# Optimization experiments

Measured on AMD Instinct MI355X. Metric: run time of the kernel, lower is better.

Reference implementation:

```python
import jax, jax.numpy as jnp
import numpy as np

VOCAB, HID, ADIM, B = 20, 128, 3, 32
NP, EP, NM, EM = 50000, 800000, 50000, 800000
IN_DIM = VOCAB + 3  # one-hot residues + 3D pos


def _gcn_conv(x, edge_index, W, b, n):
    # PyG GCNConv: h = XW; add self-loops; sym-normalized scatter-add; + bias
    h = x @ W
    loop = jnp.arange(n, dtype=edge_index.dtype)
    src = jnp.concatenate([edge_index[0], loop])
    dst = jnp.concatenate([edge_index[1], loop])
    deg = jax.ops.segment_sum(jnp.ones_like(dst, dtype=h.dtype), dst, num_segments=n)
    dinv = jnp.where(deg > 0, jax.lax.rsqrt(deg), 0.0)
    norm = dinv[src] * dinv[dst]  # [E+N]
    msg = h[src] * norm[:, None]  # [E+N, HID] dominant memory traffic
    return jax.ops.segment_sum(msg, dst, num_segments=n) + b


def _mean_pool(x, batch, nb):
    s = jax.ops.segment_sum(x, batch, num_segments=nb)
    c = jax.ops.segment_sum(jnp.ones((x.shape[0],), x.dtype), batch, num_segments=nb)
    return s / jnp.maximum(c, 1.0)[:, None]


def setup_inputs() -> dict:
    key = jax.random.key(0)
    ks = jax.random.split(key, 32)
    p = lambda k, shp: jax.random.normal(k, shp, dtype=jnp.float32) * 0.02
    inp = {
        "protein_residue": jax.random.randint(ks[0], (NP,), 0, VOCAB, dtype=jnp.int32),
        "protein_pos": jax.random.normal(ks[1], (NP, 3), dtype=jnp.float32),
        "protein_edge_index": jax.random.randint(ks[2], (2, EP), 0, NP, dtype=jnp.int32),
        "protein_batch": jnp.sort(jax.random.randint(ks[3], (NP,), 0, B, dtype=jnp.int32)),
        "molecule_residue": jax.random.randint(ks[4], (NM,), 0, VOCAB, dtype=jnp.int32),
        "molecule_pos": jax.random.normal(ks[5], (NM, 3), dtype=jnp.float32),
        "molecule_edge_index": jax.random.randint(ks[6], (2, EM), 0, NM, dtype=jnp.int32),
        "molecule_batch": jnp.sort(jax.random.randint(ks[7], (NM,), 0, B, dtype=jnp.int32)),
        "t": jax.random.randint(ks[8], (B,), 0, 1000, dtype=jnp.int32),
        "noisy_action": jax.random.normal(ks[9], (NM, ADIM), dtype=jnp.float32),
        # GCN params
        "Wp1": p(ks[10], (IN_DIM, HID)), "bp1": jnp.zeros((HID,), jnp.float32),
        "Wp2": p(ks[11], (HID, HID)),   "bp2": jnp.zeros((HID,), jnp.float32),
        "Wm1": p(ks[12], (IN_DIM, HID)), "bm1": jnp.zeros((HID,), jnp.float32),
        "Wm2": p(ks[13], (HID, HID)),   "bm2": jnp.zeros((HID,), jnp.float32),
        # timestep MLP
        "Wt1": p(ks[14], (1, HID)),   "bt1": jnp.zeros((HID,), jnp.float32),
        "Wt2": p(ks[15], (HID, HID)), "bt2": jnp.zeros((HID,), jnp.float32),
        # noise predictor: in = 2*HID + ADIM + HID = 387
        "Wn1": p(ks[16], (2 * HID + ADIM + HID, HID)), "bn1": jnp.zeros((HID,), jnp.float32),
        "Wn2": p(ks[17], (HID, ADIM)), "bn2": jnp.zeros((ADIM,), jnp.float32),
    }
    return inp


def reference(protein_residue, protein_pos, protein_edge_index, protein_batch,
              molecule_residue, molecule_pos, molecule_edge_index, molecule_batch,
              t, noisy_action,
              Wp1, bp1, Wp2, bp2, Wm1, bm1, Wm2, bm2,
              Wt1, bt1, Wt2, bt2, Wn1, bn1, Wn2, bn2):
    # protein branch
    x_p = jnp.concatenate([jax.nn.one_hot(protein_residue, VOCAB, dtype=jnp.float32), protein_pos], axis=1)
    x_p = jax.nn.relu(_gcn_conv(x_p, protein_edge_index, Wp1, bp1, NP))
    x_p = jax.nn.relu(_gcn_conv(x_p, protein_edge_index, Wp2, bp2, NP))
    protein_emb = _mean_pool(x_p, protein_batch, B)  # [B, HID]
    # molecule branch
    x_m = jnp.concatenate([jax.nn.one_hot(molecule_residue, VOCAB, dtype=jnp.float32), molecule_pos], axis=1)
    x_m = jax.nn.relu(_gcn_conv(x_m, molecule_edge_index, Wm1, bm1, NM))
    x_m = jax.nn.relu(_gcn_conv(x_m, molecule_edge_index, Wm2, bm2, NM))
    # timestep embedding
    t_emb = jax.nn.relu(t[:, None].astype(jnp.float32) @ Wt1 + bt1) @ Wt2 + bt2  # [B, HID]
    # gather pooled embeddings per molecule node, concat, MLP
    feat = jnp.concatenate([x_m, protein_emb[molecule_batch], t_emb[molecule_batch], noisy_action], axis=1)
    return jax.nn.relu(feat @ Wn1 + bn1) @ Wn2 + bn2  # [NM, ADIM]
```

## Files before the change

### kernel.cpp

```cpp
#include <hip/hip_runtime.h>
#include <hip/hip_bf16.h>

#define HID 128
#define BSH 7
#define CSRCAP 4096
#define PCHUNK 4096
#define HCHUNK 16384

typedef __attribute__((ext_vector_type(8))) short short8v;
typedef __attribute__((ext_vector_type(4))) float f32x4;

#if defined(__has_builtin)
#if __has_builtin(__builtin_amdgcn_cvt_f32_fp8) && __has_builtin(__builtin_amdgcn_cvt_pk_fp8_f32)
#define HAVE_HW_FP8 1
#endif
#endif

__device__ __forceinline__ float4 f4fma(float a, float4 x, float4 y) {
    y.x += a * x.x; y.y += a * x.y; y.z += a * x.z; y.w += a * x.w; return y;
}
__device__ __forceinline__ unsigned f2bf2(float lo, float hi) {
    unsigned ul = __float_as_uint(lo), uh = __float_as_uint(hi);
    ul = (ul + 0x7FFF + ((ul >> 16) & 1)) >> 16;
    uh = (uh + 0x7FFF + ((uh >> 16) & 1)) & 0xFFFF0000u;
    return ul | uh;
}
__device__ __forceinline__ unsigned short f2bf1(float v) {
    unsigned u = __float_as_uint(v);
    u = (u + 0x7FFF + ((u >> 16) & 1)) >> 16;
    return (unsigned short)u;
}
__device__ __forceinline__ float bflo(unsigned u) { return __uint_as_float(u << 16); }
__device__ __forceinline__ float bfhi(unsigned u) { return __uint_as_float(u & 0xFFFF0000u); }
__device__ __forceinline__ float bf2f(unsigned short b) {
    return __uint_as_float(((unsigned)b) << 16);
}
__device__ __forceinline__ short8v zero8() {
    short8v z = {0, 0, 0, 0, 0, 0, 0, 0};
    return z;
}

#ifndef HAVE_HW_FP8
__device__ __forceinline__ unsigned fp8enc_pos(float a) {
    if (a >= 448.f) return 0x7Eu;
    if (a < 0.0009765625f) return 0u;
    unsigned b = __float_as_uint(a);
    int e = (int)(b >> 23) - 127;
    if (e >= -6) {
        unsigned r = b + 0x7FFFFu + ((b >> 20) & 1u);
        e = (int)(r >> 23) - 127;
        unsigned m = (r >> 20) & 7u;
        return ((unsigned)(e + 7) << 3) | m;
    } else {
        int m = (int)(a * 512.f + 0.5f);
        return (unsigned)m;
    }
}
__device__ __forceinline__ float fp8dec1(unsigned u7) {
    float fn = __uint_as_float((u7 + 0x3C0u) << 20);
    float fs = (float)u7 * 0.001953125f;
    return u7 >= 8 ? fn : fs;
}
#endif

__device__ __forceinline__ unsigned enc4(float a, float b, float c, float d) {
#ifdef HAVE_HW_FP8
    int pk = __builtin_amdgcn_cvt_pk_fp8_f32(a, b, 0, false);
    pk = __builtin_amdgcn_cvt_pk_fp8_f32(c, d, pk, true);
    return (unsigned)pk;
#else
    return fp8enc_pos(a) | (fp8enc_pos(b) << 8) | (fp8enc_pos(c) << 16) | (fp8enc_pos(d) << 24);
#endif
}
__device__ __forceinline__ void dec8(uint2 u, float* v) {
#ifdef HAVE_HW_FP8
    v[0] = __builtin_amdgcn_cvt_f32_fp8((int)u.x, 0);
    v[1] = __builtin_amdgcn_cvt_f32_fp8((int)u.x, 1);
    v[2] = __builtin_amdgcn_cvt_f32_fp8((int)u.x, 2);
    v[3] = __builtin_amdgcn_cvt_f32_fp8((int)u.x, 3);
    v[4] = __builtin_amdgcn_cvt_f32_fp8((int)u.y, 0);
    v[5] = __builtin_amdgcn_cvt_f32_fp8((int)u.y, 1);
    v[6] = __builtin_amdgcn_cvt_f32_fp8((int)u.y, 2);
    v[7] = __builtin_amdgcn_cvt_f32_fp8((int)u.y, 3);
#else
    v[0] = fp8dec1(u.x & 0xffu);         v[1] = fp8dec1((u.x >> 8) & 0xffu);
    v[2] = fp8dec1((u.x >> 16) & 0xffu); v[3] = fp8dec1(u.x >> 24);
    v[4] = fp8dec1(u.y & 0xffu);         v[5] = fp8dec1((u.y >> 8) & 0xffu);
    v[6] = fp8dec1((u.y >> 16) & 0xffu); v[7] = fp8dec1(u.y >> 24);
#endif
}

__global__ __launch_bounds__(256) void k_bhist(const int* __restrict__ d1, int e1,
        const int* __restrict__ d2, int e2, int base2,
        int* __restrict__ bktcnt, long etot) {
    __shared__ int hist[1024];
    int tid = threadIdx.x;
    for (int b = tid; b < 1024; b += 256) hist[b] = 0;
    __syncthreads();
    long start = (long)blockIdx.x * HCHUNK;
    long end = start + HCHUNK; if (end > etot) end = etot;
    for (long i = start + tid; i < end; i += 256) {
        int d = (i < e1) ? d1[i] : d2[i - e1] + base2;
        atomicAdd(&hist[d >> BSH], 1);
    }
    __syncthreads();
    for (int b = tid; b < 1024; b += 256)
        if (hist[b]) atomicAdd(&bktcnt[b], hist[b]);
}

__global__ void k_bscan(const int* __restrict__ bktcnt, int* __restrict__ bofs,
                        int* __restrict__ bcur) {
    __shared__ int s[1024];
    int tid = threadIdx.x;
    int v = bktcnt[tid];
    s[tid] = v; __syncthreads();
    for (int o = 1; o < 1024; o <<= 1) {
        int t = (tid >= o) ? s[tid - o] : 0;
        __syncthreads();
        s[tid] += t;
        __syncthreads();
    }
    int ex = s[tid] - v;
    bofs[tid] = ex;
    bcur[tid] = ex;
    if (tid == 1023) bofs[1024] = s[1023];
}

__global__ __launch_bounds__(256) void k_part(
        const int* __restrict__ s1, const int* __restrict__ d1, int e1,
        const int* __restrict__ s2, const int* __restrict__ d2, int e2, int base2,
        int* __restrict__ bcur, int2* __restrict__ pedge, int nb, long etot) {
    __shared__ int hist[1024];
    __shared__ int lofs[1024];
    __shared__ int gb[1024];
    __shared__ int ps[256];
    __shared__ int2 stage[PCHUNK];
    __shared__ unsigned short sbk[PCHUNK];
    int tid = threadIdx.x;
    long cbase = (long)blockIdx.x * PCHUNK;
    int cnt = (int)((etot - cbase) < PCHUNK ? (etot - cbase) : PCHUNK);
    for (int b = tid; b < 1024; b += 256) hist[b] = 0;
    __syncthreads();
    for (int i = tid; i < cnt; i += 256) {
        long e = cbase + i;
        int d = (e < e1) ? d1[e] : d2[e - e1] + base2;
        atomicAdd(&hist[d >> BSH], 1);
    }
    __syncthreads();
    int h0 = hist[tid * 4], h1 = hist[tid * 4 + 1], h2 = hist[tid * 4 + 2], h3 = hist[tid * 4 + 3];
    int sum = h0 + h1 + h2 + h3;
    ps[tid] = sum; __syncthreads();
    for (int o = 1; o < 256; o <<= 1) {
        int v = (tid >= o) ? ps[tid - o] : 0;
        __syncthreads();
        ps[tid] += v;
        __syncthreads();
    }
    int ex = ps[tid] - sum;
    lofs[tid * 4] = ex; lofs[tid * 4 + 1] = ex + h0;
    lofs[tid * 4 + 2] = ex + h0 + h1; lofs[tid * 4 + 3] = ex + h0 + h1 + h2;
    __syncthreads();
    for (int b = tid; b < nb; b += 256) {
        int c = hist[b];
        gb[b] = c ? atomicAdd(&bcur[b], c) : 0;
    }
    __syncthreads();
    for (int b = tid; b < 1024; b += 256) hist[b] = 0;
    __syncthreads();
    for (int i = tid; i < cnt; i += 256) {
        long e = cbase + i;
        int s, d;
        if (e < e1) { s = s1[e]; d = d1[e]; }
        else { s = s2[e - e1] + base2; d = d2[e - e1] + base2; }
        int b = d >> BSH;
        int p = lofs[b] + atomicAdd(&hist[b], 1);
        stage[p] = make_int2(s, d);
        sbk[p] = (unsigned short)b;
    }
    __syncthreads();
    for (int i = tid; i < cnt; i += 256) {
        int b = sbk[i];
        pedge[gb[b] + (i - lofs[b])] = stage[i];
    }
}

__global__ __launch_bounds__(256) void k_csr(const int2* __restrict__ pe,
        const int* __restrict__ bofs, int* __restrict__ csrs,
        int* __restrict__ deg, int* __restrict__ offs, float* __restrict__ dinv,
        const int* __restrict__ res1, const float* __restrict__ pos1,
        const int* __restrict__ res2, const float* __restrict__ pos2,
        int np, int np64, uint4* __restrict__ nrec, int n) {
    __shared__ int lofs2[128];
    __shared__ int lcnt[128];
    __shared__ int lcur[128];
    __shared__ int sc[128];
    __shared__ int ss[CSRCAP];
    int b = blockIdx.x, tid = threadIdx.x;
    int n0 = b << BSH;
    int nn = (n - n0) < 128 ? (n - n0) : 128;
    if (tid < 128) { lcnt[tid] = 0; lcur[tid] = 0; }
    __syncthreads();
    int base = bofs[b], total = bofs[b + 1] - base;
    for (int i = tid; i < total; i += 256) atomicAdd(&lcnt[pe[base + i].y - n0], 1);
    __syncthreads();
    int v = 0;
    if (tid < 128) { v = lcnt[tid]; sc[tid] = v; }
    __syncthreads();
    for (int o = 1; o < 128; o <<= 1) {
        int t = 0;
        if (tid < 128 && tid >= o) t = sc[tid - o];
        __syncthreads();
        if (tid < 128) sc[tid] += t;
        __syncthreads();
    }
    if (tid < 128) lofs2[tid] = sc[tid] - v;
    if (tid < nn) {
        int node = n0 + tid;
        offs[node] = base + sc[tid] - v;
        deg[node] = v;
        float dv = rsqrtf((float)(v + 1));
        dinv[node] = dv;
        const int* res = 0; const float* pos = 0; int bseg = 0; bool valid = false;
        if (node < np) { res = res1; pos = pos1; bseg = 0; valid = true; }
        else if (node >= np64) { res = res2; pos = pos2; bseg = np64; valid = true; }
        if (valid) {
            int lg = node - bseg;
            uint4 rr;
            rr.x = __float_as_uint(dv);
            rr.y = (unsigned)res[lg] | ((unsigned)f2bf1(pos[lg * 3 + 0]) << 16);
            rr.z = (unsigned)f2bf1(pos[lg * 3 + 1]) | ((unsigned)f2bf1(pos[lg * 3 + 2]) << 16);
            rr.w = 0;
            nrec[node] = rr;
        }
    }
    __syncthreads();
    if (total <= CSRCAP) {
        for (int i = tid; i < total; i += 256) {
            int2 e = pe[base + i];
            int ln = e.y - n0;
            int pos_ = lofs2[ln] + atomicAdd(&lcur[ln], 1);
            ss[pos_] = e.x;
        }
        __syncthreads();
        for (int i = tid; i < total; i += 256) csrs[base + i] = ss[i];
    } else {
        for (int i = tid; i < total; i += 256) {
            int2 e = pe[base + i];
            int ln = e.y - n0;
            int pos_ = lofs2[ln] + atomicAdd(&lcur[ln], 1);
            csrs[base + pos_] = e.x;
        }
    }
}

__global__ __launch_bounds__(256) void k_agg23(
        const uint4* __restrict__ nrec, const int* __restrict__ offs,
        const int* __restrict__ deg, const int* __restrict__ csrs,
        int np, int np64, int nm,
        const float* __restrict__ W1a, const float* __restrict__ b1a,
        const float* __restrict__ W1b, const float* __restrict__ b1b,
        unsigned* __restrict__ xout) {
    __shared__ float agg[8][20];
    int grp = threadIdx.x >> 5, lane = threadIdx.x & 31;
    int g = blockIdx.x * 8 + grp;
    const float4 *W4, *bp;
    if (g < np) { W4 = (const float4*)W1a; bp = (const float4*)b1a; }
    else if (g >= np64 && g < np64 + nm) { W4 = (const float4*)W1b; bp = (const float4*)b1b; }
    else return;
    if (lane < 20) agg[grp][lane] = 0.f;
    float sx = 0.f, sy = 0.f, sz = 0.f;
    int s0 = offs[g], m = deg[g];
    for (int i = lane; i < m; i += 32) {
        int s = csrs[s0 + i];
        uint4 r = nrec[s];
        float dv = __uint_as_float(r.x);
        int rs = (int)(r.y & 0xffffu);
        float px = bfhi(r.y);
        float py = bflo(r.z);
        float pz = bfhi(r.z);
        atomicAdd(&agg[grp][rs], dv);
        sx += dv * px; sy += dv * py; sz += dv * pz;
    }
    #pragma unroll
    for (int o = 1; o < 32; o <<= 1) {
        sx += __shfl_xor(sx, o, 32);
        sy += __shfl_xor(sy, o, 32);
        sz += __shfl_xor(sz, o, 32);
    }
    uint4 sr = nrec[g];
    float dd = __uint_as_float(sr.x);
    int rsd = (int)(sr.y & 0xffffu);
    float spx = bfhi(sr.y), spy = bflo(sr.z), spz = bfhi(sr.z);
    float4 w20 = W4[20 * 32 + lane], w21 = W4[21 * 32 + lane], w22 = W4[22 * 32 + lane];
    float4 sm = W4[rsd * 32 + lane];
    sm = f4fma(spx, w20, sm); sm = f4fma(spy, w21, sm); sm = f4fma(spz, w22, sm);
    float4 acc = make_float4(dd * sm.x, dd * sm.y, dd * sm.z, dd * sm.w);
    #pragma unroll
    for (int r = 0; r < 20; ++r)
        acc = f4fma(agg[grp][r], W4[r * 32 + lane], acc);
    acc = f4fma(sx, w20, acc);
    acc = f4fma(sy, w21, acc);
    acc = f4fma(sz, w22, acc);
    float4 b = bp[lane];
    float s16 = 16.f * dd;
    float o0 = s16 * fmaxf(dd * acc.x + b.x, 0.f);
    float o1 = s16 * fmaxf(dd * acc.y + b.y, 0.f);
    float o2 = s16 * fmaxf(dd * acc.z + b.z, 0.f);
    float o3 = s16 * fmaxf(dd * acc.w + b.w, 0.f);
    xout[(size_t)g * 32 + lane] = enc4(o0, o1, o2, o3);
}

__global__ __launch_bounds__(256) void k_agg(
        const uint2* __restrict__ H8, const int* __restrict__ offs,
        const int* __restrict__ deg, const int* __restrict__ csrs,
        const float* __restrict__ dinv,
        int np, int np64, int nm,
        unsigned short* __restrict__ outb) {
    int g = blockIdx.x * 8 + (threadIdx.x >> 5);
    if (g >= np && (g < np64 || g >= np64 + nm)) return;
    int lane = threadIdx.x & 31;
    int half = lane >> 4, l15 = lane & 15;
    float acc[8];
    if (half == 0) {
        uint2 u = H8[(size_t)g * 16 + l15];
        float v[8]; dec8(u, v);
        #pragma unroll
        for (int c = 0; c < 8; ++c) acc[c] = v[c];
    } else {
        #pragma unroll
        for (int c = 0; c < 8; ++c) acc[c] = 0.f;
    }
    int s0 = offs[g], m = deg[g];
    int npair = (m + 1) >> 1;
    #pragma unroll 8
    for (int j = 0; j < npair; ++j) {
        int idx = 2 * j + half;
        bool act = idx < m;
        int s = csrs[s0 + (act ? idx : m - 1)];
        uint2 u = H8[(size_t)s * 16 + l15];
        float v[8]; dec8(u, v);
        if (act) {
            #pragma unroll
            for (int c = 0; c < 8; ++c) acc[c] += v[c];
        }
    }
    #pragma unroll
    for (int c = 0; c < 8; ++c) acc[c] += __shfl_xor(acc[c], 16, 32);
    if (half == 0) {
        float di = dinv[g] * 0.0625f;
        uint4 pk;
        pk.x = f2bf2(di * acc[0], di * acc[1]);
        pk.y = f2bf2(di * acc[2], di * acc[3]);
        pk.z = f2bf2(di * acc[4], di * acc[5]);
        pk.w = f2bf2(di * acc[6], di * acc[7]);
        *(uint4*)&outb[(size_t)g * HID + l15 * 8] = pk;
    }
}

__global__ void k_tr(const float* __restrict__ Wa, const float* __restrict__ Wb,
                     const float* __restrict__ Wc,
                     unsigned short* __restrict__ Ta, unsigned short* __restrict__ Tb,
                     unsigned short* __restrict__ Tc) {
    int b = blockIdx.x;
    int col = b & 127, m = b >> 7;
    const float* W = (m == 0) ? Wa : (m == 1 ? Wb : Wc);
    unsigned short* T = (m == 0) ? Ta : (m == 1 ? Tb : Tc);
    int k = threadIdx.x;
    T[col * HID + k] = f2bf1(W[k * HID + col]);
}

__global__ __launch_bounds__(256) void k_gemm(const unsigned short* __restrict__ A,
        const unsigned short* __restrict__ Bt1, const unsigned short* __restrict__ Bt2,
        const float* __restrict__ b2a, const float* __restrict__ b2b,
        int nb1, int np64, int ntot, unsigned short* __restrict__ C) {
    const int tid = threadIdx.x;
    const int wid = tid >> 6;
    const int lane = tid & 63;
    const int l15 = lane & 15, lg = lane >> 4;
    const unsigned short* Bt; const float* bb; int r0;
    if ((int)blockIdx.x < nb1) { Bt = Bt1; bb = b2a; r0 = blockIdx.x * 64; }
    else { Bt = Bt2; bb = b2b; r0 = np64 + ((int)blockIdx.x - nb1) * 64; }
    const int cbase = wid * 32;
    f32x4 acc[4][2] = {};
    #pragma unroll
    for (int ks = 0; ks < 4; ++ks) {
        int kb = ks * 32 + lg * 8;
        short8v b0 = *(const short8v*)&Bt[(size_t)(cbase + l15) * HID + kb];
        short8v b1 = *(const short8v*)&Bt[(size_t)(cbase + 16 + l15) * HID + kb];
        #pragma unroll
        for (int rt = 0; rt < 4; ++rt) {
            int gr = r0 + rt * 16 + l15;
            short8v a = (gr < ntot) ? *(const short8v*)&A[(size_t)gr * HID + kb] : zero8();
            acc[rt][0] = __builtin_amdgcn_mfma_f32_16x16x32_bf16(a, b0, acc[rt][0], 0, 0, 0);
            acc[rt][1] = __builtin_amdgcn_mfma_f32_16x16x32_bf16(a, b1, acc[rt][1], 0, 0, 0);
        }
    }
    float bc0 = bb[cbase + l15], bc1 = bb[cbase + 16 + l15];
    #pragma unroll
    for (int rt = 0; rt < 4; ++rt)
        #pragma unroll
        for (int i = 0; i < 4; ++i) {
            int gr = r0 + rt * 16 + lg * 4 + i;
            if (gr < ntot) {
                C[(size_t)gr * HID + cbase + l15]      = f2bf1(fmaxf(acc[rt][0][i] + bc0, 0.f));
                C[(size_t)gr * HID + cbase + 16 + l15] = f2bf1(fmaxf(acc[rt][1][i] + bc1, 0.f));
            }
        }
}

__global__ void k_pool(const unsigned short* __restrict__ x, const int* __restrict__ batch,
                       float* __restrict__ pool, int* __restrict__ cnt, int n) {
    const int ROWS = 64;
    int start = blockIdx.x * ROWS;
    if (start >= n) return;
    int end = start + ROWS; if (end > n) end = n;
    int c = threadIdx.x;
    float acc = 0.f;
    int cur = batch[start];
    int run = 0;
    for (int r = start; r < end; ++r) {
        int b = batch[r];
        if (b != cur) {
            atomicAdd(&pool[cur * HID + c], acc);
            if (c == 0) atomicAdd(&cnt[cur], run);
            acc = 0.f; run = 0; cur = b;
        }
        acc += bf2f(x[(size_t)r * HID + c]);
        run++;
    }
    atomicAdd(&pool[cur * HID + c], acc);
    if (c == 0) atomicAdd(&cnt[cur], run);
}

__global__ void k_combo2(const int* __restrict__ t, const float* __restrict__ Wt1,
                         const float* __restrict__ bt1, const float* __restrict__ Wt2,
                         const float* __restrict__ bt2,
                         const float* __restrict__ pool, const int* __restrict__ cntb,
                         const float* __restrict__ Wn1, const float* __restrict__ bn1,
                         float* __restrict__ combo) {
    __shared__ float th[HID];
    __shared__ float pe[HID];
    __shared__ float te[HID];
    int b = blockIdx.x, c = threadIdx.x;
    float tv = (float)t[b];
    float hv = tv * Wt1[c] + bt1[c];
    th[c] = hv > 0.f ? hv : 0.f;
    float dcnt = (float)cntb[b]; if (dcnt < 1.f) dcnt = 1.f;
    pe[c] = pool[b * HID + c] / dcnt;
    __syncthreads();
    float s = bt2[c];
    for (int k = 0; k < HID; ++k) s += th[k] * Wt2[k * HID + c];
    te[c] = s;
    __syncthreads();
    const float* Wp = Wn1 + 128 * HID;
    const float* Wt = Wn1 + 256 * HID;
    float o = bn1[c];
    for (int k = 0; k < HID; ++k)
        o += pe[k] * Wp[k * HID + c] + te[k] * Wt[k * HID + c];
    combo[b * HID + c] = o;
}

__global__ __launch_bounds__(256) void k_final(const unsigned short* __restrict__ A,
        const unsigned short* __restrict__ Bt ,
        const float* __restrict__ Wn1, const float* __restrict__ combo,
        const int* __restrict__ mbatch, const float* __restrict__ noisy,
        const float* __restrict__ Wn2, const float* __restrict__ bn2,
        float* __restrict__ out, int n) {
    __shared__ float hsm[64][132];
    const int tid = threadIdx.x;
    const int wid = tid >> 6;
    const int lane = tid & 63;
    const int l15 = lane & 15, lg = lane >> 4;
    const int r0 = blockIdx.x * 64;
    const int cbase = wid * 32;
    f32x4 acc[4][2] = {};
    #pragma unroll
    for (int ks = 0; ks < 4; ++ks) {
        int kb = ks * 32 + lg * 8;
        short8v b0 = *(const short8v*)&Bt[(size_t)(cbase + l15) * HID + kb];
        short8v b1 = *(const short8v*)&Bt[(size_t)(cbase + 16 + l15) * HID + kb];
        #pragma unroll
        for (int rt = 0; rt < 4; ++rt) {
            int gr = r0 + rt * 16 + l15;
            short8v a = (gr < n) ? *(const short8v*)&A[(size_t)gr * HID + kb] : zero8();
            acc[rt][0] = __builtin_amdgcn_mfma_f32_16x16x32_bf16(a, b0, acc[rt][0], 0, 0, 0);
            acc[rt][1] = __builtin_amdgcn_mfma_f32_16x16x32_bf16(a, b1, acc[rt][1], 0, 0, 0);
        }
    }
    const float* Wna = Wn1 + 384 * HID;
    #pragma unroll
    for (int rt = 0; rt < 4; ++rt)
        #pragma unroll
        for (int i = 0; i < 4; ++i) {
            int lr = rt * 16 + lg * 4 + i;
            int gr = r0 + lr;
            if (gr < n) {
                int b = mbatch[gr];
                float na0 = noisy[gr * 3 + 0], na1 = noisy[gr * 3 + 1], na2 = noisy[gr * 3 + 2];
                #pragma unroll
                for (int ct = 0; ct < 2; ++ct) {
                    int col = cbase + ct * 16 + l15;
                    float v = acc[rt][ct][i]
                            + na0 * Wna[col] + na1 * Wna[HID + col] + na2 * Wna[2 * HID + col]
                            + combo[b * HID + col];
                    hsm[lr][col] = v > 0.f ? v : 0.f;
                }
            }
        }
    __syncthreads();
    if (tid < 192) {
        int lr = tid / 3, j = tid - lr * 3;
        int gr = r0 + lr;
        if (gr < n) {
            float s = bn2[j];
            for (int c = 0; c < HID; ++c) s += hsm[lr][c] * Wn2[c * 3 + j];
            out[(size_t)gr * 3 + j] = s;
        }
    }
}

extern "C" void kernel_launch(void* const* d_in, const int* in_sizes, int n_in,
                              void* d_out, int out_size, void* d_ws, size_t ws_size,
                              hipStream_t stream) {
    const int*   p_res  = (const int*)d_in[0];
    const float* p_pos  = (const float*)d_in[1];
    const int*   p_ei   = (const int*)d_in[2];
    const int*   p_bat  = (const int*)d_in[3];
    const int*   m_res  = (const int*)d_in[4];
    const float* m_pos  = (const float*)d_in[5];
    const int*   m_ei   = (const int*)d_in[6];
    const int*   m_bat  = (const int*)d_in[7];
    const int*   t      = (const int*)d_in[8];
    const float* noisy  = (const float*)d_in[9];
    const float* Wp1 = (const float*)d_in[10], *bp1 = (const float*)d_in[11];
    const float* Wp2 = (const float*)d_in[12], *bp2 = (const float*)d_in[13];
    const float* Wm1 = (const float*)d_in[14], *bm1 = (const float*)d_in[15];
    const float* Wm2 = (const float*)d_in[16], *bm2 = (const float*)d_in[17];
    const float* Wt1 = (const float*)d_in[18], *bt1 = (const float*)d_in[19];
    const float* Wt2 = (const float*)d_in[20], *bt2 = (const float*)d_in[21];
    const float* Wn1 = (const float*)d_in[22], *bn1 = (const float*)d_in[23];
    const float* Wn2 = (const float*)d_in[24], *bn2 = (const float*)d_in[25];
    float* out = (float*)d_out;

    const int NP = in_sizes[0];
    const int EP = in_sizes[2] / 2;
    const int NM = in_sizes[4];
    const int EM = in_sizes[6] / 2;
    const int B  = in_sizes[8];
    auto al64 = [](int x) { return (x + 63) & ~63; };

    const int np64 = al64(NP);
    const long ntot_m = (long)np64 + NM;
    const long e2sum = (long)EP + EM;

    auto align256 = [](size_t x) { return (x + 255) & ~(size_t)255; };
    size_t req = 0;
    auto count = [&](size_t nb) { req = align256(req) + nb; };
    count(4ull * ntot_m);
    count(4ull * ntot_m);
    count(4ull * ntot_m);
    count(16ull * ntot_m);
    count(4ull * (1024 + 1025 + 1024));
    count(8ull * e2sum);
    count(4ull * e2sum);
    count(1ull * ntot_m * HID);
    count(2ull * ntot_m * HID);
    count(2ull * ntot_m * HID);
    count(2ull * 3 * HID * HID);
    count(4ull * (size_t)B * (HID + 1));
    count(4ull * (size_t)B * HID);
    bool merged = ws_size >= req + 4096;

    char* ws = (char*)d_ws;
    size_t off = 0;
    auto alloc = [&](size_t nb) { off = align256(off); size_t r = off; off += nb; return r; };

    const int NMAX = NP > NM ? NP : NM;
    const int EMAXs = EP > EM ? EP : EM;
    const long ntot_a = merged ? ntot_m : (long)al64(NMAX);
    const long etot_a = merged ? e2sum : (long)EMAXs;

    int*   deg  = (int*)(ws + alloc(4ull * ntot_a));
    int*   offs = (int*)(ws + alloc(4ull * ntot_a));
    float* dinv = (float*)(ws + alloc(4ull * ntot_a));
    uint4* nrec = (uint4*)(ws + alloc(16ull * ntot_a));
    int*   bktcnt = (int*)(ws + alloc(4ull * (1024 + 1025 + 1024)));
    int*   bofs = bktcnt + 1024;
    int*   bcur = bofs + 1025;
    int2*  csre = (int2*)(ws + alloc(8ull * etot_a));
    int*   csrs = (int*)(ws + alloc(4ull * etot_a));
    unsigned* hb8 = (unsigned*)(ws + alloc(1ull * ntot_a * HID));
    unsigned short* hb = (unsigned short*)(ws + alloc(2ull * ntot_a * HID));
    unsigned short* hc = (unsigned short*)(ws + alloc(2ull * ntot_a * HID));
    unsigned short* w2ta = (unsigned short*)(ws + alloc(2ull * 3 * HID * HID));
    unsigned short* w2tb = w2ta + HID * HID;
    unsigned short* wn1t = w2ta + 2 * HID * HID;
    float* pool = (float*)(ws + alloc(4ull * (size_t)B * (HID + 1)));
    int*   cntb = (int*)(pool + (size_t)B * HID);
    float* combo = (float*)(ws + alloc(4ull * (size_t)B * HID));

    k_tr<<<384, HID, 0, stream>>>(Wp2, Wm2, Wn1, w2ta, w2tb, wn1t);

    auto run = [&](int np_, int nm_,
                   const int* ei1, int e1, const int* ei2, int e2,
                   const int* res1, const float* pos1, const int* res2, const float* pos2,
                   const float* W1a, const float* b1a, const float* W1b, const float* b1b,
                   const float* b2a, const float* b2b) {
        const int np64_ = al64(np_);
        const int ntot = np64_ + nm_;
        const long etot = (long)e1 + e2;
        const int nb = (ntot + 127) >> BSH;
        const int* s1 = ei1, *d1 = ei1 + e1;
        const int* s2 = ei2, *d2 = ei2 + e2;
        hipMemsetAsync(bktcnt, 0, 4096, stream);
        k_bhist<<<(int)((etot + HCHUNK - 1) / HCHUNK), 256, 0, stream>>>(
            d1, e1, d2, e2, np64_, bktcnt, etot);
        k_bscan<<<1, 1024, 0, stream>>>(bktcnt, bofs, bcur);
        k_part<<<(int)((etot + PCHUNK - 1) / PCHUNK), 256, 0, stream>>>(
            s1, d1, e1, s2, d2, e2, np64_, bcur, csre, nb, etot);
        k_csr<<<nb, 256, 0, stream>>>(csre, bofs, csrs, deg, offs, dinv,
                                      res1, pos1, res2, pos2, np_, np64_, nrec, ntot);
        k_agg23<<<(ntot + 7) / 8, 256, 0, stream>>>(nrec, offs, deg, csrs,
                                                    np_, np64_, nm_,
                                                    W1a, b1a, W1b, b1b, hb8);
        k_agg<<<(ntot + 7) / 8, 256, 0, stream>>>((const uint2*)hb8, offs, deg, csrs, dinv,
                                                  np_, np64_, nm_, hc);
        const int nb1 = np64_ / 64;
        const int nb2 = (nm_ + 63) / 64;
        k_gemm<<<nb1 + nb2, 256, 0, stream>>>(hc, w2ta, w2tb, b2a, b2b, nb1, np64_, ntot, hb);
    };

    if (merged) {
        run(NP, NM, p_ei, EP, m_ei, EM,
            p_res, p_pos, m_res, m_pos,
            Wp1, bp1, Wm1, bm1, bp2, bm2);
        hipMemsetAsync(pool, 0, 4ull * (size_t)B * (HID + 1), stream);
        k_pool<<<(NP + 63) / 64, HID, 0, stream>>>(hb, p_bat, pool, cntb, NP);
        k_combo2<<<B, HID, 0, stream>>>(t, Wt1, bt1, Wt2, bt2, pool, cntb, Wn1, bn1, combo);
        k_final<<<(NM + 63) / 64, 256, 0, stream>>>(hb + (size_t)np64 * HID, wn1t, Wn1, combo,
                                                    m_bat, noisy, Wn2, bn2, out, NM);
    } else {
        run(NP, 0, p_ei, EP, p_ei, 0,
            p_res, p_pos, p_res, p_pos,
            Wp1, bp1, Wp1, bp1, bp2, bp2);
        hipMemsetAsync(pool, 0, 4ull * (size_t)B * (HID + 1), stream);
        k_pool<<<(NP + 63) / 64, HID, 0, stream>>>(hb, p_bat, pool, cntb, NP);
        k_combo2<<<B, HID, 0, stream>>>(t, Wt1, bt1, Wt2, bt2, pool, cntb, Wn1, bn1, combo);
        run(0, NM, m_ei, 0, m_ei, EM,
            m_res, m_pos, m_res, m_pos,
            Wm1, bm1, Wm1, bm1, bm2, bm2);
        k_final<<<(NM + 63) / 64, 256, 0, stream>>>(hb, wn1t, Wn1, combo, m_bat, noisy,
                                                    Wn2, bn2, out, NM);
    }
}
```

Baseline: 274.5 us.

## Pack partitioned edges into one int and widen fp8 aggregation to 16B loads

The partition stage now stores each edge as a single int, holding the source shifted left plus the destination's low bits within its bucket. This halves the partitioned-edge buffer and its write and read traffic in the CSR build. The fp8 aggregation kernel now has 8 lanes per row, each loading 16 bytes, so four neighbors are processed per warp step instead of two. Neighbor indices are loaded 32 at a time and broadcast with shuffles, which cuts redundant index loads but adds a second shuffle-reduction stage and more registers. The packing assumes source indices fit in 25 bits, which holds for the merged node counts here.

Result: faster. 240.7 us (-12.3%).

```diff
diff --git a/kernel.cpp b/kernel.cpp
--- a/kernel.cpp
+++ b/kernel.cpp
@@ -72,22 +72,19 @@
     return fp8enc_pos(a) | (fp8enc_pos(b) << 8) | (fp8enc_pos(c) << 16) | (fp8enc_pos(d) << 24);
 #endif
 }
-__device__ __forceinline__ void dec8(uint2 u, float* v) {
+__device__ __forceinline__ void dec4(unsigned x, float* v) {
 #ifdef HAVE_HW_FP8
-    v[0] = __builtin_amdgcn_cvt_f32_fp8((int)u.x, 0);
-    v[1] = __builtin_amdgcn_cvt_f32_fp8((int)u.x, 1);
-    v[2] = __builtin_amdgcn_cvt_f32_fp8((int)u.x, 2);
-    v[3] = __builtin_amdgcn_cvt_f32_fp8((int)u.x, 3);
-    v[4] = __builtin_amdgcn_cvt_f32_fp8((int)u.y, 0);
-    v[5] = __builtin_amdgcn_cvt_f32_fp8((int)u.y, 1);
-    v[6] = __builtin_amdgcn_cvt_f32_fp8((int)u.y, 2);
-    v[7] = __builtin_amdgcn_cvt_f32_fp8((int)u.y, 3);
+    v[0] = __builtin_amdgcn_cvt_f32_fp8((int)x, 0);
+    v[1] = __builtin_amdgcn_cvt_f32_fp8((int)x, 1);
+    v[2] = __builtin_amdgcn_cvt_f32_fp8((int)x, 2);
+    v[3] = __builtin_amdgcn_cvt_f32_fp8((int)x, 3);
 #else
-    v[0] = fp8dec1(u.x & 0xffu);         v[1] = fp8dec1((u.x >> 8) & 0xffu);
-    v[2] = fp8dec1((u.x >> 16) & 0xffu); v[3] = fp8dec1(u.x >> 24);
-    v[4] = fp8dec1(u.y & 0xffu);         v[5] = fp8dec1((u.y >> 8) & 0xffu);
-    v[6] = fp8dec1((u.y >> 16) & 0xffu); v[7] = fp8dec1(u.y >> 24);
+    v[0] = fp8dec1(x & 0xffu);         v[1] = fp8dec1((x >> 8) & 0xffu);
+    v[2] = fp8dec1((x >> 16) & 0xffu); v[3] = fp8dec1(x >> 24);
 #endif
+}
+__device__ __forceinline__ void dec16(uint4 u, float* v) {
+    dec4(u.x, v); dec4(u.y, v + 4); dec4(u.z, v + 8); dec4(u.w, v + 12);
 }
 
 __global__ __launch_bounds__(256) void k_bhist(const int* __restrict__ d1, int e1,
@@ -129,12 +126,12 @@
 __global__ __launch_bounds__(256) void k_part(
         const int* __restrict__ s1, const int* __restrict__ d1, int e1,
         const int* __restrict__ s2, const int* __restrict__ d2, int e2, int base2,
-        int* __restrict__ bcur, int2* __restrict__ pedge, int nb, long etot) {
+        int* __restrict__ bcur, int* __restrict__ pedge, int nb, long etot) {
     __shared__ int hist[1024];
     __shared__ int lofs[1024];
     __shared__ int gb[1024];
     __shared__ int ps[256];
-    __shared__ int2 stage[PCHUNK];
+    __shared__ int stage[PCHUNK];
     __shared__ unsigned short sbk[PCHUNK];
     int tid = threadIdx.x;
     long cbase = (long)blockIdx.x * PCHUNK;
@@ -174,7 +171,7 @@
         else { s = s2[e - e1] + base2; d = d2[e - e1] + base2; }
         int b = d >> BSH;
         int p = lofs[b] + atomicAdd(&hist[b], 1);
-        stage[p] = make_int2(s, d);
+        stage[p] = (s << BSH) | (d & ((1 << BSH) - 1));
         sbk[p] = (unsigned short)b;
     }
     __syncthreads();
@@ -184,7 +181,7 @@
     }
 }
 
-__global__ __launch_bounds__(256) void k_csr(const int2* __restrict__ pe,
+__global__ __launch_bounds__(256) void k_csr(const int* __restrict__ pe,
         const int* __restrict__ bofs, int* __restrict__ csrs,
         int* __restrict__ deg, int* __restrict__ offs, float* __restrict__ dinv,
         const int* __restrict__ res1, const float* __restrict__ pos1,
@@ -201,7 +198,8 @@
     if (tid < 128) { lcnt[tid] = 0; lcur[tid] = 0; }
     __syncthreads();
     int base = bofs[b], total = bofs[b + 1] - base;
-    for (int i = tid; i < total; i += 256) atomicAdd(&lcnt[pe[base + i].y - n0], 1);
+    for (int i = tid; i < total; i += 256)
+        atomicAdd(&lcnt[pe[base + i] & ((1 << BSH) - 1)], 1);
     __syncthreads();
     int v = 0;
     if (tid < 128) { v = lcnt[tid]; sc[tid] = v; }
@@ -236,19 +234,19 @@
     __syncthreads();
     if (total <= CSRCAP) {
         for (int i = tid; i < total; i += 256) {
-            int2 e = pe[base + i];
-            int ln = e.y - n0;
+            int e = pe[base + i];
+            int ln = e & ((1 << BSH) - 1);
             int pos_ = lofs2[ln] + atomicAdd(&lcur[ln], 1);
-            ss[pos_] = e.x;
+            ss[pos_] = e >> BSH;
         }
         __syncthreads();
         for (int i = tid; i < total; i += 256) csrs[base + i] = ss[i];
     } else {
         for (int i = tid; i < total; i += 256) {
-            int2 e = pe[base + i];
-            int ln = e.y - n0;
+            int e = pe[base + i];
+            int ln = e & ((1 << BSH) - 1);
             int pos_ = lofs2[ln] + atomicAdd(&lcur[ln], 1);
-            csrs[base + pos_] = e.x;
+            csrs[base + pos_] = e >> BSH;
         }
     }
 }
@@ -311,7 +309,7 @@
 }
 
 __global__ __launch_bounds__(256) void k_agg(
-        const uint2* __restrict__ H8, const int* __restrict__ offs,
+        const uint4* __restrict__ H8, const int* __restrict__ offs,
         const int* __restrict__ deg, const int* __restrict__ csrs,
         const float* __restrict__ dinv,
         int np, int np64, int nm,
@@ -319,41 +317,52 @@
     int g = blockIdx.x * 8 + (threadIdx.x >> 5);
     if (g >= np && (g < np64 || g >= np64 + nm)) return;
     int lane = threadIdx.x & 31;
-    int half = lane >> 4, l15 = lane & 15;
-    float acc[8];
-    if (half == 0) {
-        uint2 u = H8[(size_t)g * 16 + l15];
-        float v[8]; dec8(u, v);
-        #pragma unroll
-        for (int c = 0; c < 8; ++c) acc[c] = v[c];
+    int q = lane >> 3, l8 = lane & 7;
+    float acc[16];
+    if (q == 0) {
+        uint4 u = H8[(size_t)g * 8 + l8];
+        dec16(u, acc);
     } else {
         #pragma unroll
-        for (int c = 0; c < 8; ++c) acc[c] = 0.f;
+        for (int c = 0; c < 16; ++c) acc[c] = 0.f;
     }
     int s0 = offs[g], m = deg[g];
-    int npair = (m + 1) >> 1;
-    #pragma unroll 8
-    for (int j = 0; j < npair; ++j) {
-        int idx = 2 * j + half;
-        bool act = idx < m;
-        int s = csrs[s0 + (act ? idx : m - 1)];
-        uint2 u = H8[(size_t)s * 16 + l15];
-        float v[8]; dec8(u, v);
-        if (act) {
-            #pragma unroll
-            for (int c = 0; c < 8; ++c) acc[c] += v[c];
+    for (int c0 = 0; c0 < m; c0 += 32) {
+        int rem = m - c0; if (rem > 32) rem = 32;
+        int li = lane < rem ? lane : rem - 1;
+        int se = csrs[s0 + c0 + li];
+        int nquad = (rem + 3) >> 2;
+        #pragma unroll 8
+        for (int j = 0; j < nquad; ++j) {
+            int idx = j * 4 + q;
+            bool act = idx < rem;
+            int s = __shfl(se, act ? idx : 0, 32);
+            uint4 u = H8[(size_t)s * 8 + l8];
+            if (act) {
+                float v[16]; dec16(u, v);
+                #pragma unroll
+                for (int c = 0; c < 16; ++c) acc[c] += v[c];
+            }
         }
     }
     #pragma unroll
-    for (int c = 0; c < 8; ++c) acc[c] += __shfl_xor(acc[c], 16, 32);
-    if (half == 0) {
+    for (int c = 0; c < 16; ++c) {
+        acc[c] += __shfl_xor(acc[c], 8, 32);
+        acc[c] += __shfl_xor(acc[c], 16, 32);
+    }
+    if (q == 0) {
         float di = dinv[g] * 0.0625f;
-        uint4 pk;
-        pk.x = f2bf2(di * acc[0], di * acc[1]);
-        pk.y = f2bf2(di * acc[2], di * acc[3]);
-        pk.z = f2bf2(di * acc[4], di * acc[5]);
-        pk.w = f2bf2(di * acc[6], di * acc[7]);
-        *(uint4*)&outb[(size_t)g * HID + l15 * 8] = pk;
+        uint4 pk0, pk1;
+        pk0.x = f2bf2(di * acc[0],  di * acc[1]);
+        pk0.y = f2bf2(di * acc[2],  di * acc[3]);
+        pk0.z = f2bf2(di * acc[4],  di * acc[5]);
+        pk0.w = f2bf2(di * acc[6],  di * acc[7]);
+        pk1.x = f2bf2(di * acc[8],  di * acc[9]);
+        pk1.y = f2bf2(di * acc[10], di * acc[11]);
+        pk1.z = f2bf2(di * acc[12], di * acc[13]);
+        pk1.w = f2bf2(di * acc[14], di * acc[15]);
+        *(uint4*)&outb[(size_t)g * HID + l8 * 16]     = pk0;
+        *(uint4*)&outb[(size_t)g * HID + l8 * 16 + 8] = pk1;
     }
 }
 
@@ -561,7 +570,7 @@
     count(4ull * ntot_m);
     count(16ull * ntot_m);
     count(4ull * (1024 + 1025 + 1024));
-    count(8ull * e2sum);
+    count(4ull * e2sum);
     count(4ull * e2sum);
     count(1ull * ntot_m * HID);
     count(2ull * ntot_m * HID);
@@ -587,7 +596,7 @@
     int*   bktcnt = (int*)(ws + alloc(4ull * (1024 + 1025 + 1024)));
     int*   bofs = bktcnt + 1024;
     int*   bcur = bofs + 1025;
-    int2*  csre = (int2*)(ws + alloc(8ull * etot_a));
+    int*   csre = (int*)(ws + alloc(4ull * etot_a));
     int*   csrs = (int*)(ws + alloc(4ull * etot_a));
     unsigned* hb8 = (unsigned*)(ws + alloc(1ull * ntot_a * HID));
     unsigned short* hb = (unsigned short*)(ws + alloc(2ull * ntot_a * HID));
@@ -623,7 +632,7 @@
         k_agg23<<<(ntot + 7) / 8, 256, 0, stream>>>(nrec, offs, deg, csrs,
                                                     np_, np64_, nm_,
                                                     W1a, b1a, W1b, b1b, hb8);
-        k_agg<<<(ntot + 7) / 8, 256, 0, stream>>>((const uint2*)hb8, offs, deg, csrs, dinv,
+        k_agg<<<(ntot + 7) / 8, 256, 0, stream>>>((const uint4*)hb8, offs, deg, csrs, dinv,
                                                   np_, np64_, nm_, hc);
         const int nb1 = np64_ / 64;
         const int nb2 = (nm_ + 63) / 64;
```
